# Optimization experiments

Measured on AMD Instinct MI355X. Metric: run time of the kernel, lower is better.

The kernel has to match this reference:

```python
import jax, jax.numpy as jnp
import numpy as np

NUM_FREQS = 8
TEMPERATURE = 100.0
DOWNSAMPLE = 64
GRID = 8
D_OUT = 512


def fourier_embed(x):
    # x: [M, 2] -> [M, NUM_FREQS*2*2], order: per freq [sin(f*x), cos(f*x)]
    freqs = TEMPERATURE ** (jnp.arange(NUM_FREQS, dtype=jnp.float32) / NUM_FREQS)
    xf = x[:, None, :] * freqs[None, :, None]  # [M, F, 2]
    feats = jnp.stack([jnp.sin(xf), jnp.cos(xf)], axis=2)  # [M, F, 2, 2]
    return feats.reshape(x.shape[0], -1)  # [M, 32]


def mlp(x, W1, b1, W2, b2, W3, b3):
    h = jax.nn.silu(x @ W1 + b1)
    h = jax.nn.silu(h @ W2 + b2)
    return h @ W3 + b3


def scatter_to_grid(drags, emb):
    # drags: [BV, N, 2] (pixel coords), emb: [BV, N, 512]
    BV, N, _ = drags.shape
    r = drags[..., 0].astype(jnp.int32) // DOWNSAMPLE  # [BV, N]
    c = drags[..., 1].astype(jnp.int32) // DOWNSAMPLE
    idx = r * GRID + c  # flat cell index in [0, 64)
    b_idx = jnp.arange(BV)[:, None]
    grid = jnp.zeros((BV, GRID * GRID, D_OUT), emb.dtype).at[b_idx, idx].add(emb)
    # -> [BV, 512, 8, 8]
    return grid.transpose(0, 2, 1).reshape(BV, D_OUT, GRID, GRID)


def setup_inputs() -> dict:
    key = jax.random.key(0)
    ks = jax.random.split(key, 8)
    B, V, N = 8, 8, 1024
    IMG = GRID * DOWNSAMPLE  # 512
    drags_start = jax.random.uniform(ks[0], (B, V, N, 2), jnp.float32) * IMG
    drags_end = jax.random.uniform(ks[1], (B, V, N, 2), jnp.float32) * IMG
    pd = NUM_FREQS * 2 * 2  # 32
    W1 = jax.random.normal(ks[2], (pd, 128), jnp.float32) * (1.0 / np.sqrt(pd))
    b1 = jnp.zeros((128,), jnp.float32)
    W2 = jax.random.normal(ks[3], (128, 256), jnp.float32) * (1.0 / np.sqrt(128))
    b2 = jnp.zeros((256,), jnp.float32)
    W3 = jax.random.normal(ks[4], (256, 512), jnp.float32) * (1.0 / np.sqrt(256))
    b3 = jnp.zeros((512,), jnp.float32)
    return dict(drags_start=drags_start, drags_end=drags_end,
                W1=W1, b1=b1, W2=W2, b2=b2, W3=W3, b3=b3)


def reference(drags_start, drags_end, W1, b1, W2, b2, W3, b3):
    B, V, N, _ = drags_start.shape
    BV = B * V
    ds = drags_start.reshape(BV, N, 2)
    de = drags_end.reshape(BV, N, 2)

    def embed(d):  # [BV, N, 2] -> [BV, N, 512]
        feats = fourier_embed(d.reshape(BV * N, 2))  # no_grad in torch
        return mlp(feats, W1, b1, W2, b2, W3, b3).reshape(BV, N, D_OUT)

    emb_s = embed(ds)
    emb_e = embed(de)
    merge_s = scatter_to_grid(ds, emb_s)
    merge_e = scatter_to_grid(de, emb_e)
    return jnp.concatenate([merge_s, merge_e], axis=1)  # [BV, 1024, 8, 8]
```

## Files before the change

### kernel.cpp

```cpp
#include <hip/hip_runtime.h>
#include <hip/hip_bf16.h>

typedef _Float16 half8 __attribute__((ext_vector_type(8)));
typedef _Float16 half4v __attribute__((ext_vector_type(4)));
typedef float floatx4 __attribute__((ext_vector_type(4)));
typedef unsigned int uint2v __attribute__((ext_vector_type(2)));

__device__ const float FREQS[8] = {
    1.0f, 1.7782794100389228f, 3.1622776601683795f, 5.623413251903491f,
    10.0f, 17.78279410038923f, 31.622776601683793f, 56.23413251903491f};

__device__ inline void fsincos(float m, float& s, float& c) {
  constexpr double I2PI_D = 0.15915494309189533576888376337251;
  constexpr float HI = (float)I2PI_D;
  constexpr float LO = (float)(I2PI_D - (double)HI);
  float k = rintf(m * HI);
  float f = fmaf(m, HI, -k);
  f = fmaf(m, LO, f);
  s = __builtin_amdgcn_sinf(f);
  c = __builtin_amdgcn_cosf(f);
}

__device__ inline float fsilu(float x) {
  return x * __builtin_amdgcn_rcpf(1.f + __expf(-x));
}

__global__ __launch_bounds__(512, 4) void embed_scatter(
    const float* __restrict__ dstart, const float* __restrict__ dend,
    const float* __restrict__ W1, const float* __restrict__ b1,
    const float* __restrict__ W2, const float* __restrict__ b2,
    const float* __restrict__ W3, _Float16* __restrict__ W3f,
    _Float16* __restrict__ swz, int* __restrict__ counts) {
  __shared__ _Float16 smem[16384 + 4096];
  _Float16* h1f = smem;
  _Float16* W1lds = smem + 16384;
  _Float16* h2t = smem;
  __shared__ float b1lds[128];
  __shared__ unsigned char cellb[256];
  __shared__ int hist[64];

  int bid = blockIdx.x;
  int bv = bid >> 3, tsel = (bid >> 2) & 1, pg = bid & 3;
  const float* src = tsel ? dend : dstart;
  int tid = threadIdx.x;
  int lane = tid & 63, w = tid >> 6, ln = lane & 15, q = lane >> 4;

  if (tid < 32) {
    int t = bid * 32 + tid;
    int lnn = t & 15, qq = (t >> 4) & 3, ks = (t >> 6) & 7, I = t >> 9;
    half8 v;
    for (int j = 0; j < 8; j++)
      v[j] = (_Float16)W3[(size_t)(ks * 32 + qq * 8 + j) * 512 + I * 16 + lnn];
    *(half8*)&W3f[(size_t)t * 8] = v;
  }

  {
    int n = tid >> 2, kb = (tid & 3) * 8;
    half8 v;
    for (int j = 0; j < 8; j++) v[j] = (_Float16)W1[(kb + j) * 128 + n];
    *(half8*)&W1lds[n * 32 + kb] = v;
  }
  if (tid < 128) b1lds[tid] = b1[tid];
  if (tid < 64) hist[tid] = 0;
  __syncthreads();

  int pbase = bv * 1024 + pg * 256;
  if (tid < 256) {
    float2 xy = *(const float2*)&src[(size_t)(pbase + tid) * 2];
    int cell = ((int)xy.x >> 6) * 8 + ((int)xy.y >> 6);
    cellb[tid] = (unsigned char)cell;
    atomicAdd(&hist[cell], 1);
  }

  half8 w2f[2][4];
  float b2v[2];
  for (int nt = 0; nt < 2; nt++) {
    int n = w * 32 + nt * 16 + ln;
    b2v[nt] = b2[n];
    for (int ks = 0; ks < 4; ks++) {
      half8 v;
      for (int j = 0; j < 8; j++)
        v[j] = (_Float16)W2[(ks * 32 + q * 8 + j) * 256 + n];
      w2f[nt][ks] = v;
    }
  }
  floatx4 sacc[4][2];
  for (int mc = 0; mc < 4; mc++)
    for (int nt = 0; nt < 2; nt++) sacc[mc][nt] = (floatx4){0.f, 0.f, 0.f, 0.f};

  float fA = FREQS[2 * q], fB = FREQS[2 * q + 1];
  __syncthreads();

  for (int c = 0; c < 2; c++) {
    int pl = c * 128 + w * 16 + ln;
    float2 xy = *(const float2*)&src[(size_t)(pbase + pl) * 2];
    half8 fb;
    {
      float s, cc2;
      fsincos(xy.x * fA, s, cc2); fb[0] = (_Float16)s; fb[2] = (_Float16)cc2;
      fsincos(xy.y * fA, s, cc2); fb[1] = (_Float16)s; fb[3] = (_Float16)cc2;
      fsincos(xy.x * fB, s, cc2); fb[4] = (_Float16)s; fb[6] = (_Float16)cc2;
      fsincos(xy.y * fB, s, cc2); fb[5] = (_Float16)s; fb[7] = (_Float16)cc2;
    }
    for (int mtW = 0; mtW < 8; mtW++) {
      half8 w1f = *(const half8*)&W1lds[(mtW * 16 + ln) * 32 + q * 8];
      floatx4 c1 = *(const floatx4*)&b1lds[mtW * 16 + q * 4];
      c1 = __builtin_amdgcn_mfma_f32_16x16x32_f16(w1f, fb, c1, 0, 0, 0);
      half4v hv;
      for (int r = 0; r < 4; r++) hv[r] = (_Float16)fsilu(c1[r]);
      int addr = (((w * 4 + (mtW >> 1)) * 4 + ((mtW & 1) * 2 + (q >> 1))) * 16 + ln) * 8 + (q & 1) * 4;
      *(half4v*)&h1f[addr] = hv;
    }
    __syncthreads();
    for (int tt = 0; tt < 8; tt++) {
      half8 af[4];
      for (int ks = 0; ks < 4; ks++)
        af[ks] = *(const half8*)&h1f[(((tt * 4 + ks) * 4 + q) * 16 + ln) * 8];
      unsigned ca = *(const unsigned*)&cellb[c * 128 + tt * 16 + q * 4];
      unsigned e0 = ca & 255, e1 = (ca >> 8) & 255, e2 = (ca >> 16) & 255, e3 = ca >> 24;
      half4v oh[4];
      for (int mc = 0; mc < 4; mc++) {
        unsigned m = (unsigned)(mc * 16 + ln);
        unsigned d0 = (e0 == m ? 0x3C00u : 0u) | (e1 == m ? 0x3C000000u : 0u);
        unsigned d1 = (e2 == m ? 0x3C00u : 0u) | (e3 == m ? 0x3C000000u : 0u);
        uint2v u = {d0, d1};
        oh[mc] = __builtin_bit_cast(half4v, u);
      }
      for (int nt = 0; nt < 2; nt++) {
        floatx4 cc = {b2v[nt], b2v[nt], b2v[nt], b2v[nt]};
        for (int ks = 0; ks < 4; ks++)
          cc = __builtin_amdgcn_mfma_f32_16x16x32_f16(af[ks], w2f[nt][ks], cc, 0, 0, 0);
        half4v hb;
        for (int r = 0; r < 4; r++) hb[r] = (_Float16)fsilu(cc[r]);
        for (int mc = 0; mc < 4; mc++)
          sacc[mc][nt] = __builtin_amdgcn_mfma_f32_16x16x16f16(oh[mc], hb, sacc[mc][nt], 0, 0, 0);
      }
    }
    __syncthreads();
  }

  for (int mc = 0; mc < 4; mc++)
    for (int nt = 0; nt < 2; nt++)
      for (int r = 0; r < 4; r++)
        h2t[(mc * 16 + q * 4 + r) * 264 + w * 32 + nt * 16 + ln] =
            (_Float16)sacc[mc][nt][r];
  __syncthreads();
  for (int i = 0; i < 4; i++) {
    int g = i * 512 + tid;
    int lnn = g & 15, qq = (g >> 4) & 3, ks2 = (g >> 6) & 7, cn = g >> 9;
    half8 v = *(const half8*)&h2t[(cn * 16 + lnn) * 264 + ks2 * 32 + qq * 8];
    *(half8*)&swz[(size_t)bid * 16384 + (size_t)g * 8] = v;
  }
  if (tid < 64) counts[bid * 64 + tid] = hist[tid];
}

__global__ __launch_bounds__(256) void layer3(
    const _Float16* __restrict__ swz, const int* __restrict__ counts,
    const _Float16* __restrict__ W3f, const float* __restrict__ b3,
    float* __restrict__ out) {
  __shared__ _Float16 blds[16384];
  __shared__ float cnt_s[64];
  int bvts = blockIdx.x;
  int ch = blockIdx.y;
  int tid = threadIdx.x;
  const _Float16* sb = swz + (size_t)bvts * 65536;
  for (int i = 0; i < 8; i++) {
    int g = i * 256 + tid;
    half8 v0 = *(const half8*)&sb[(size_t)g * 8];
    half8 v1 = *(const half8*)&sb[16384 + (size_t)g * 8];
    half8 v2 = *(const half8*)&sb[32768 + (size_t)g * 8];
    half8 v3 = *(const half8*)&sb[49152 + (size_t)g * 8];
    *(half8*)&blds[g * 8] = (v0 + v1) + (v2 + v3);
  }
  if (tid < 64) {
    int base = bvts * 256 + tid;
    cnt_s[tid] = (float)(counts[base] + counts[base + 64] +
                         counts[base + 128] + counts[base + 192]);
  }
  __syncthreads();
  int lane = tid & 63, w = tid >> 6, ln = lane & 15, q = lane >> 4;
  floatx4 acc[4][4];
  for (int i2 = 0; i2 < 4; i2++)
    for (int cn = 0; cn < 4; cn++) acc[i2][cn] = (floatx4){0.f, 0.f, 0.f, 0.f};
  for (int ks = 0; ks < 8; ks++) {
    half8 bf[4];
    for (int cn = 0; cn < 4; cn++)
      bf[cn] = *(const half8*)&blds[(((cn * 8 + ks) * 4 + q) * 16 + ln) * 8];
    for (int i2 = 0; i2 < 4; i2++) {
      int I = ch * 16 + w * 4 + i2;
      half8 wf = *(const half8*)&W3f[(size_t)((I * 8 + ks) * 64 + lane) * 8];
      for (int cn = 0; cn < 4; cn++)
        acc[i2][cn] = __builtin_amdgcn_mfma_f32_16x16x32_f16(wf, bf[cn], acc[i2][cn], 0, 0, 0);
    }
  }
  for (int i2 = 0; i2 < 4; i2++) {
    int nb = ch * 256 + (w * 4 + i2) * 16;
    floatx4 b3v = *(const floatx4*)&b3[nb + q * 4];
    for (int cn = 0; cn < 4; cn++) {
      float cf = cnt_s[cn * 16 + ln];
      for (int r = 0; r < 4; r++)
        out[((size_t)bvts * 512 + nb + q * 4 + r) * 64 + cn * 16 + ln] =
            acc[i2][cn][r] + cf * b3v[r];
    }
  }
}

extern "C" void kernel_launch(void* const* d_in, const int* in_sizes, int n_in,
                              void* d_out, int out_size, void* d_ws, size_t ws_size,
                              hipStream_t stream) {
  const float* dstart = (const float*)d_in[0];
  const float* dend = (const float*)d_in[1];
  const float* W1 = (const float*)d_in[2];
  const float* b1 = (const float*)d_in[3];
  const float* W2 = (const float*)d_in[4];
  const float* b2 = (const float*)d_in[5];
  const float* W3 = (const float*)d_in[6];
  const float* b3 = (const float*)d_in[7];
  float* out = (float*)d_out;

  char* ws = (char*)d_ws;
  _Float16* W3f = (_Float16*)(ws);
  _Float16* swz = (_Float16*)(ws + 262144);
  int* counts = (int*)(ws + 262144 + 16777216);

  hipLaunchKernelGGL(embed_scatter, dim3(512), dim3(512), 0, stream,
                     dstart, dend, W1, b1, W2, b2, W3, W3f, swz, counts);
  hipLaunchKernelGGL(layer3, dim3(128, 2), dim3(256), 0, stream,
                     swz, counts, W3f, b3, out);
}
```

Baseline: 124.2 us.

## Double-buffer layer-1 output, overlap layers, use K=32 scatter MFMA, widen layer3

The embed kernel now keeps two LDS buffers for the layer-1 activations. Layer 2 plus scatter for the first 128 points runs while layer 1 of the second half is computed, which removes one barrier-separated phase. The scatter step now packs two 16-point tiles into one 16x16x32 MFMA instead of two 16x16x16 ones, halving the scatter MFMA count at the cost of more live registers. layer3 uses 512 threads per block with half the tiles per wave, raising parallelism per block. LDS use grows to about 72KB, which may reduce how many blocks fit per CU.

```diff
diff --git a/kernel.cpp b/kernel.cpp
--- a/kernel.cpp
+++ b/kernel.cpp
@@ -4,7 +4,7 @@
 typedef _Float16 half8 __attribute__((ext_vector_type(8)));
 typedef _Float16 half4v __attribute__((ext_vector_type(4)));
 typedef float floatx4 __attribute__((ext_vector_type(4)));
-typedef unsigned int uint2v __attribute__((ext_vector_type(2)));
+typedef unsigned int uint4v __attribute__((ext_vector_type(4)));
 
 __device__ const float FREQS[8] = {
     1.0f, 1.7782794100389228f, 3.1622776601683795f, 5.623413251903491f,
@@ -31,9 +31,10 @@
     const float* __restrict__ W2, const float* __restrict__ b2,
     const float* __restrict__ W3, _Float16* __restrict__ W3f,
     _Float16* __restrict__ swz, int* __restrict__ counts) {
-  __shared__ _Float16 smem[16384 + 4096];
-  _Float16* h1f = smem;
-  _Float16* W1lds = smem + 16384;
+  __shared__ _Float16 smem[36864];
+  _Float16* h1f0 = smem;
+  _Float16* h1f1 = smem + 16384;
+  _Float16* W1lds = smem + 32768;
   _Float16* h2t = smem;
   __shared__ float b1lds[128];
   __shared__ unsigned char cellb[256];
@@ -53,7 +54,6 @@
       v[j] = (_Float16)W3[(size_t)(ks * 32 + qq * 8 + j) * 512 + I * 16 + lnn];
     *(half8*)&W3f[(size_t)t * 8] = v;
   }
-
   {
     int n = tid >> 2, kb = (tid & 3) * 8;
     half8 v;
@@ -89,55 +89,87 @@
     for (int nt = 0; nt < 2; nt++) sacc[mc][nt] = (floatx4){0.f, 0.f, 0.f, 0.f};
 
   float fA = FREQS[2 * q], fB = FREQS[2 * q + 1];
-  __syncthreads();
-
-  for (int c = 0; c < 2; c++) {
-    int pl = c * 128 + w * 16 + ln;
-    float2 xy = *(const float2*)&src[(size_t)(pbase + pl) * 2];
-    half8 fb;
-    {
-      float s, cc2;
-      fsincos(xy.x * fA, s, cc2); fb[0] = (_Float16)s; fb[2] = (_Float16)cc2;
-      fsincos(xy.y * fA, s, cc2); fb[1] = (_Float16)s; fb[3] = (_Float16)cc2;
-      fsincos(xy.x * fB, s, cc2); fb[4] = (_Float16)s; fb[6] = (_Float16)cc2;
-      fsincos(xy.y * fB, s, cc2); fb[5] = (_Float16)s; fb[7] = (_Float16)cc2;
-    }
-    for (int mtW = 0; mtW < 8; mtW++) {
-      half8 w1f = *(const half8*)&W1lds[(mtW * 16 + ln) * 32 + q * 8];
-      floatx4 c1 = *(const floatx4*)&b1lds[mtW * 16 + q * 4];
-      c1 = __builtin_amdgcn_mfma_f32_16x16x32_f16(w1f, fb, c1, 0, 0, 0);
-      half4v hv;
-      for (int r = 0; r < 4; r++) hv[r] = (_Float16)fsilu(c1[r]);
-      int addr = (((w * 4 + (mtW >> 1)) * 4 + ((mtW & 1) * 2 + (q >> 1))) * 16 + ln) * 8 + (q & 1) * 4;
-      *(half4v*)&h1f[addr] = hv;
-    }
-    __syncthreads();
-    for (int tt = 0; tt < 8; tt++) {
-      half8 af[4];
-      for (int ks = 0; ks < 4; ks++)
-        af[ks] = *(const half8*)&h1f[(((tt * 4 + ks) * 4 + q) * 16 + ln) * 8];
-      unsigned ca = *(const unsigned*)&cellb[c * 128 + tt * 16 + q * 4];
-      unsigned e0 = ca & 255, e1 = (ca >> 8) & 255, e2 = (ca >> 16) & 255, e3 = ca >> 24;
-      half4v oh[4];
-      for (int mc = 0; mc < 4; mc++) {
-        unsigned m = (unsigned)(mc * 16 + ln);
-        unsigned d0 = (e0 == m ? 0x3C00u : 0u) | (e1 == m ? 0x3C000000u : 0u);
-        unsigned d1 = (e2 == m ? 0x3C00u : 0u) | (e3 == m ? 0x3C000000u : 0u);
-        uint2v u = {d0, d1};
-        oh[mc] = __builtin_bit_cast(half4v, u);
-      }
-      for (int nt = 0; nt < 2; nt++) {
-        floatx4 cc = {b2v[nt], b2v[nt], b2v[nt], b2v[nt]};
-        for (int ks = 0; ks < 4; ks++)
-          cc = __builtin_amdgcn_mfma_f32_16x16x32_f16(af[ks], w2f[nt][ks], cc, 0, 0, 0);
-        half4v hb;
-        for (int r = 0; r < 4; r++) hb[r] = (_Float16)fsilu(cc[r]);
-        for (int mc = 0; mc < 4; mc++)
-          sacc[mc][nt] = __builtin_amdgcn_mfma_f32_16x16x16f16(oh[mc], hb, sacc[mc][nt], 0, 0, 0);
-      }
-    }
-    __syncthreads();
-  }
+  float2 xy0 = *(const float2*)&src[(size_t)(pbase + w * 16 + ln) * 2];
+  float2 xy1 = *(const float2*)&src[(size_t)(pbase + 128 + w * 16 + ln) * 2];
+
+#define FEATS(xy, fb)                                                     \
+  {                                                                       \
+    float s_, c_;                                                         \
+    fsincos((xy).x * fA, s_, c_); fb[0] = (_Float16)s_; fb[2] = (_Float16)c_; \
+    fsincos((xy).y * fA, s_, c_); fb[1] = (_Float16)s_; fb[3] = (_Float16)c_; \
+    fsincos((xy).x * fB, s_, c_); fb[4] = (_Float16)s_; fb[6] = (_Float16)c_; \
+    fsincos((xy).y * fB, s_, c_); fb[5] = (_Float16)s_; fb[7] = (_Float16)c_; \
+  }
+
+#define LAYER1(fb, dst)                                                   \
+  for (int mtW = 0; mtW < 8; mtW++) {                                     \
+    half8 w1f = *(const half8*)&W1lds[(mtW * 16 + ln) * 32 + q * 8];      \
+    floatx4 c1 = *(const floatx4*)&b1lds[mtW * 16 + q * 4];               \
+    c1 = __builtin_amdgcn_mfma_f32_16x16x32_f16(w1f, fb, c1, 0, 0, 0);    \
+    half4v hv;                                                            \
+    for (int r = 0; r < 4; r++) hv[r] = (_Float16)fsilu(c1[r]);           \
+    int addr = (((w * 4 + (mtW >> 1)) * 4 + ((mtW & 1) * 2 + (q >> 1))) * 16 + ln) * 8 + (q & 1) * 4; \
+    *(half4v*)&(dst)[addr] = hv;                                          \
+  }
+
+#define LAYER2SC(c, buf)                                                  \
+  for (int t = 0; t < 4; t++) {                                           \
+    half8 af[4];                                                          \
+    floatx4 ce[2];                                                        \
+    half4v he[2];                                                         \
+    for (int ks = 0; ks < 4; ks++)                                        \
+      af[ks] = *(const half8*)&(buf)[((((2 * t) * 4 + ks) * 4 + q) * 16 + ln) * 8]; \
+    for (int nt = 0; nt < 2; nt++) {                                      \
+      ce[nt] = (floatx4){b2v[nt], b2v[nt], b2v[nt], b2v[nt]};             \
+      for (int ks = 0; ks < 4; ks++)                                      \
+        ce[nt] = __builtin_amdgcn_mfma_f32_16x16x32_f16(af[ks], w2f[nt][ks], ce[nt], 0, 0, 0); \
+      for (int r = 0; r < 4; r++) he[nt][r] = (_Float16)fsilu(ce[nt][r]); \
+    }                                                                     \
+    for (int ks = 0; ks < 4; ks++)                                        \
+      af[ks] = *(const half8*)&(buf)[((((2 * t + 1) * 4 + ks) * 4 + q) * 16 + ln) * 8]; \
+    unsigned ca = *(const unsigned*)&cellb[(c) * 128 + t * 32 + q * 4];   \
+    unsigned cb = *(const unsigned*)&cellb[(c) * 128 + t * 32 + 16 + q * 4]; \
+    unsigned a0 = ca & 255, a1 = (ca >> 8) & 255, a2 = (ca >> 16) & 255, a3 = ca >> 24; \
+    unsigned e0 = cb & 255, e1 = (cb >> 8) & 255, e2 = (cb >> 16) & 255, e3 = cb >> 24; \
+    half8 oh[4];                                                          \
+    for (int mc = 0; mc < 4; mc++) {                                      \
+      unsigned m = (unsigned)(mc * 16 + ln);                              \
+      uint4v u;                                                           \
+      u[0] = (a0 == m ? 0x3C00u : 0u) | (a1 == m ? 0x3C000000u : 0u);     \
+      u[1] = (a2 == m ? 0x3C00u : 0u) | (a3 == m ? 0x3C000000u : 0u);     \
+      u[2] = (e0 == m ? 0x3C00u : 0u) | (e1 == m ? 0x3C000000u : 0u);     \
+      u[3] = (e2 == m ? 0x3C00u : 0u) | (e3 == m ? 0x3C000000u : 0u);     \
+      oh[mc] = __builtin_bit_cast(half8, u);                              \
+    }                                                                     \
+    for (int nt = 0; nt < 2; nt++) {                                      \
+      floatx4 co = (floatx4){b2v[nt], b2v[nt], b2v[nt], b2v[nt]};         \
+      for (int ks = 0; ks < 4; ks++)                                      \
+        co = __builtin_amdgcn_mfma_f32_16x16x32_f16(af[ks], w2f[nt][ks], co, 0, 0, 0); \
+      half8 hb;                                                           \
+      for (int r = 0; r < 4; r++) {                                       \
+        hb[r] = he[nt][r];                                                \
+        hb[4 + r] = (_Float16)fsilu(co[r]);                               \
+      }                                                                   \
+      for (int mc = 0; mc < 4; mc++)                                      \
+        sacc[mc][nt] = __builtin_amdgcn_mfma_f32_16x16x32_f16(oh[mc], hb, sacc[mc][nt], 0, 0, 0); \
+    }                                                                     \
+  }
+
+  {
+    half8 fb0;
+    FEATS(xy0, fb0)
+    LAYER1(fb0, h1f0)
+  }
+  __syncthreads();
+  {
+    half8 fb1;
+    FEATS(xy1, fb1)
+    LAYER2SC(0, h1f0)
+    LAYER1(fb1, h1f1)
+  }
+  __syncthreads();
+  LAYER2SC(1, h1f1)
+  __syncthreads();
 
   for (int mc = 0; mc < 4; mc++)
     for (int nt = 0; nt < 2; nt++)
@@ -154,7 +186,7 @@
   if (tid < 64) counts[bid * 64 + tid] = hist[tid];
 }
 
-__global__ __launch_bounds__(256) void layer3(
+__global__ __launch_bounds__(512) void layer3(
     const _Float16* __restrict__ swz, const int* __restrict__ counts,
     const _Float16* __restrict__ W3f, const float* __restrict__ b3,
     float* __restrict__ out) {
@@ -164,8 +196,8 @@
   int ch = blockIdx.y;
   int tid = threadIdx.x;
   const _Float16* sb = swz + (size_t)bvts * 65536;
-  for (int i = 0; i < 8; i++) {
-    int g = i * 256 + tid;
+  for (int i = 0; i < 4; i++) {
+    int g = i * 512 + tid;
     half8 v0 = *(const half8*)&sb[(size_t)g * 8];
     half8 v1 = *(const half8*)&sb[16384 + (size_t)g * 8];
     half8 v2 = *(const half8*)&sb[32768 + (size_t)g * 8];
@@ -179,22 +211,22 @@
   }
   __syncthreads();
   int lane = tid & 63, w = tid >> 6, ln = lane & 15, q = lane >> 4;
-  floatx4 acc[4][4];
-  for (int i2 = 0; i2 < 4; i2++)
+  floatx4 acc[2][4];
+  for (int i2 = 0; i2 < 2; i2++)
     for (int cn = 0; cn < 4; cn++) acc[i2][cn] = (floatx4){0.f, 0.f, 0.f, 0.f};
   for (int ks = 0; ks < 8; ks++) {
     half8 bf[4];
     for (int cn = 0; cn < 4; cn++)
       bf[cn] = *(const half8*)&blds[(((cn * 8 + ks) * 4 + q) * 16 + ln) * 8];
-    for (int i2 = 0; i2 < 4; i2++) {
-      int I = ch * 16 + w * 4 + i2;
+    for (int i2 = 0; i2 < 2; i2++) {
+      int I = ch * 16 + w * 2 + i2;
       half8 wf = *(const half8*)&W3f[(size_t)((I * 8 + ks) * 64 + lane) * 8];
       for (int cn = 0; cn < 4; cn++)
         acc[i2][cn] = __builtin_amdgcn_mfma_f32_16x16x32_f16(wf, bf[cn], acc[i2][cn], 0, 0, 0);
     }
   }
-  for (int i2 = 0; i2 < 4; i2++) {
-    int nb = ch * 256 + (w * 4 + i2) * 16;
+  for (int i2 = 0; i2 < 2; i2++) {
+    int nb = ch * 256 + (w * 2 + i2) * 16;
     floatx4 b3v = *(const floatx4*)&b3[nb + q * 4];
     for (int cn = 0; cn < 4; cn++) {
       float cf = cnt_s[cn * 16 + ln];
@@ -225,6 +257,6 @@
 
   hipLaunchKernelGGL(embed_scatter, dim3(512), dim3(512), 0, stream,
                      dstart, dend, W1, b1, W2, b2, W3, W3f, swz, counts);
-  hipLaunchKernelGGL(layer3, dim3(128, 2), dim3(256), 0, stream,
+  hipLaunchKernelGGL(layer3, dim3(128, 2), dim3(512), 0, stream,
                      swz, counts, W3f, b3, out);
 }
```

After: 127.5 us. 1.03x slower.

## Fuse layer3 into embed_scatter using last-block-done atomic counters

Applied to the files above, without the earlier changes.

Removes the separate layer3 kernel. The last of each group of four embed blocks, detected with a threadfence plus an atomic counter, reduces the four partial grids and runs the W3 GEMM for all 512 output channels itself. W3 conversion and flag reset move to a small prep kernel launched first. This overlaps layer3 work with the tail of the embed phase and avoids one dependent-launch boundary. In exchange it adds a launch, halves the number of blocks doing the layer3 GEMM, and raises register pressure inside a kernel bounded at 512 threads with 4 blocks per CU.

```diff
diff --git a/kernel.cpp b/kernel.cpp
--- a/kernel.cpp
+++ b/kernel.cpp
@@ -25,34 +25,41 @@
   return x * __builtin_amdgcn_rcpf(1.f + __expf(-x));
 }
 
+__global__ __launch_bounds__(256) void prep_w3(const float* __restrict__ W3,
+                                               _Float16* __restrict__ W3f,
+                                               int* __restrict__ flags) {
+  int t = blockIdx.x * 256 + threadIdx.x;
+  if (t < 128) flags[t] = 0;
+  int ln = t & 15, q = (t >> 4) & 3, ks = (t >> 6) & 7, I = t >> 9;
+  half8 v;
+  for (int j = 0; j < 8; j++)
+    v[j] = (_Float16)W3[(size_t)(ks * 32 + q * 8 + j) * 512 + I * 16 + ln];
+  *(half8*)&W3f[(size_t)t * 8] = v;
+}
+
 __global__ __launch_bounds__(512, 4) void embed_scatter(
     const float* __restrict__ dstart, const float* __restrict__ dend,
     const float* __restrict__ W1, const float* __restrict__ b1,
     const float* __restrict__ W2, const float* __restrict__ b2,
-    const float* __restrict__ W3, _Float16* __restrict__ W3f,
-    _Float16* __restrict__ swz, int* __restrict__ counts) {
+    const _Float16* __restrict__ W3f, const float* __restrict__ b3,
+    _Float16* __restrict__ swz, int* __restrict__ counts,
+    int* __restrict__ flags, float* __restrict__ out) {
   __shared__ _Float16 smem[16384 + 4096];
   _Float16* h1f = smem;
   _Float16* W1lds = smem + 16384;
   _Float16* h2t = smem;
+  _Float16* blds = smem;
   __shared__ float b1lds[128];
+  __shared__ float cnt_s[64];
   __shared__ unsigned char cellb[256];
   __shared__ int hist[64];
+  __shared__ int isLast;
 
   int bid = blockIdx.x;
   int bv = bid >> 3, tsel = (bid >> 2) & 1, pg = bid & 3;
   const float* src = tsel ? dend : dstart;
   int tid = threadIdx.x;
   int lane = tid & 63, w = tid >> 6, ln = lane & 15, q = lane >> 4;
-
-  if (tid < 32) {
-    int t = bid * 32 + tid;
-    int lnn = t & 15, qq = (t >> 4) & 3, ks = (t >> 6) & 7, I = t >> 9;
-    half8 v;
-    for (int j = 0; j < 8; j++)
-      v[j] = (_Float16)W3[(size_t)(ks * 32 + qq * 8 + j) * 512 + I * 16 + lnn];
-    *(half8*)&W3f[(size_t)t * 8] = v;
-  }
 
   {
     int n = tid >> 2, kb = (tid & 3) * 8;
@@ -152,33 +159,34 @@
     *(half8*)&swz[(size_t)bid * 16384 + (size_t)g * 8] = v;
   }
   if (tid < 64) counts[bid * 64 + tid] = hist[tid];
-}
-
-__global__ __launch_bounds__(256) void layer3(
-    const _Float16* __restrict__ swz, const int* __restrict__ counts,
-    const _Float16* __restrict__ W3f, const float* __restrict__ b3,
-    float* __restrict__ out) {
-  __shared__ _Float16 blds[16384];
-  __shared__ float cnt_s[64];
-  int bvts = blockIdx.x;
-  int ch = blockIdx.y;
-  int tid = threadIdx.x;
-  const _Float16* sb = swz + (size_t)bvts * 65536;
-  for (int i = 0; i < 8; i++) {
-    int g = i * 256 + tid;
-    half8 v0 = *(const half8*)&sb[(size_t)g * 8];
-    half8 v1 = *(const half8*)&sb[16384 + (size_t)g * 8];
-    half8 v2 = *(const half8*)&sb[32768 + (size_t)g * 8];
-    half8 v3 = *(const half8*)&sb[49152 + (size_t)g * 8];
-    *(half8*)&blds[g * 8] = (v0 + v1) + (v2 + v3);
+
+  __syncthreads();
+  if (tid == 0) {
+    __threadfence();
+    int t = atomicAdd(&flags[bid >> 2], 1);
+    isLast = (t == 3);
+  }
+  __syncthreads();
+  if (!isLast) return;
+  __threadfence();
+
+  int grp = bid >> 2;
+  const _Float16* sb = swz + (size_t)grp * 65536;
+  for (int i = 0; i < 4; i++) {
+    int e = i * 512 + tid;
+    half8 v0 = *(const half8*)&sb[(size_t)e * 8];
+    half8 v1 = *(const half8*)&sb[16384 + (size_t)e * 8];
+    half8 v2 = *(const half8*)&sb[32768 + (size_t)e * 8];
+    half8 v3 = *(const half8*)&sb[49152 + (size_t)e * 8];
+    *(half8*)&blds[e * 8] = (v0 + v1) + (v2 + v3);
   }
   if (tid < 64) {
-    int base = bvts * 256 + tid;
+    int base = grp * 256 + tid;
     cnt_s[tid] = (float)(counts[base] + counts[base + 64] +
                          counts[base + 128] + counts[base + 192]);
   }
   __syncthreads();
-  int lane = tid & 63, w = tid >> 6, ln = lane & 15, q = lane >> 4;
+
   floatx4 acc[4][4];
   for (int i2 = 0; i2 < 4; i2++)
     for (int cn = 0; cn < 4; cn++) acc[i2][cn] = (floatx4){0.f, 0.f, 0.f, 0.f};
@@ -187,19 +195,19 @@
     for (int cn = 0; cn < 4; cn++)
       bf[cn] = *(const half8*)&blds[(((cn * 8 + ks) * 4 + q) * 16 + ln) * 8];
     for (int i2 = 0; i2 < 4; i2++) {
-      int I = ch * 16 + w * 4 + i2;
+      int I = w * 4 + i2;
       half8 wf = *(const half8*)&W3f[(size_t)((I * 8 + ks) * 64 + lane) * 8];
       for (int cn = 0; cn < 4; cn++)
         acc[i2][cn] = __builtin_amdgcn_mfma_f32_16x16x32_f16(wf, bf[cn], acc[i2][cn], 0, 0, 0);
     }
   }
   for (int i2 = 0; i2 < 4; i2++) {
-    int nb = ch * 256 + (w * 4 + i2) * 16;
+    int nb = (w * 4 + i2) * 16;
     floatx4 b3v = *(const floatx4*)&b3[nb + q * 4];
     for (int cn = 0; cn < 4; cn++) {
       float cf = cnt_s[cn * 16 + ln];
       for (int r = 0; r < 4; r++)
-        out[((size_t)bvts * 512 + nb + q * 4 + r) * 64 + cn * 16 + ln] =
+        out[((size_t)grp * 512 + nb + q * 4 + r) * 64 + cn * 16 + ln] =
             acc[i2][cn][r] + cf * b3v[r];
     }
   }
@@ -222,9 +230,10 @@
   _Float16* W3f = (_Float16*)(ws);
   _Float16* swz = (_Float16*)(ws + 262144);
   int* counts = (int*)(ws + 262144 + 16777216);
-
+  int* flags = (int*)(ws + 262144 + 16777216 + 131072);
+
+  hipLaunchKernelGGL(prep_w3, dim3(64), dim3(256), 0, stream, W3, W3f, flags);
   hipLaunchKernelGGL(embed_scatter, dim3(512), dim3(512), 0, stream,
-                     dstart, dend, W1, b1, W2, b2, W3, W3f, swz, counts);
-  hipLaunchKernelGGL(layer3, dim3(128, 2), dim3(256), 0, stream,
-                     swz, counts, W3f, b3, out);
-}
+                     dstart, dend, W1, b1, W2, b2, W3f, b3, swz, counts,
+                     flags, out);
+}
```

Result: slower. 183.2 us (+47.5%).
